# Kernel optimization log

Measured on AMD Instinct MI355X. Metric: run time of the kernel, lower is better.

The kernel has to match this reference:

```python
import jax, jax.numpy as jnp
import numpy as np

IN_F = 1024
OUT_F = 1024
GRID = 8
TOKENS = 8192


def setup_inputs() -> dict:
    key = jax.random.key(0)
    k_x, k_w, k_b, k_s = jax.random.split(key, 4)
    x = jax.random.normal(k_x, (TOKENS, IN_F), dtype=jnp.float32)
    # kaiming_uniform_(nonlinearity='linear'): bound = sqrt(3/fan_in)
    bound_w = float(np.sqrt(3.0 / IN_F))
    W = jax.random.uniform(k_w, (OUT_F, IN_F), minval=-bound_w, maxval=bound_w, dtype=jnp.float32)
    # nn.Linear default bias init: U(-1/sqrt(fan_in), 1/sqrt(fan_in))
    bound_b = float(1.0 / np.sqrt(IN_F))
    b = jax.random.uniform(k_b, (OUT_F,), minval=-bound_b, maxval=bound_b, dtype=jnp.float32)
    spline_weight = jax.random.uniform(k_s, (OUT_F, IN_F, GRID), minval=-0.1, maxval=0.1, dtype=jnp.float32)
    grid = jnp.linspace(-3.0, 3.0, GRID, dtype=jnp.float32)
    return {"x": x, "W": W, "b": b, "spline_weight": spline_weight, "grid": grid}


def reference(x, W, b, spline_weight, grid):
    grid_size = spline_weight.shape[-1]
    # base path: Linear(silu(x))
    base = jnp.einsum('ti,oi->to', jax.nn.silu(x), W) + b
    # RBF basis: [tokens, in_features, grid_size]
    denom = 2.0 / (grid_size - 1) + 1e-05
    basis = jnp.exp(-(((x[..., None] - grid) / denom) ** 2))
    spline = jnp.einsum('tig,oig->to', basis, spline_weight)
    return base + spline
```

## Files before the change

kernel.cpp:

```cpp
#include <hip/hip_runtime.h>
#include <hip/hip_bf16.h>

#define IN_F   1024
#define OUT_F  1024
#define GRID_N 8
#define TOKENS 8192
#define KTOT   9216
#define KHALF  4608
#define NTILE  72

typedef __attribute__((ext_vector_type(8))) short  bf16x8;
typedef __attribute__((ext_vector_type(4))) float  f32x4;

struct TrueT  { static constexpr bool value = true;  };
struct FalseT { static constexpr bool value = false; };

__device__ __forceinline__ unsigned int f2bf(float f) {
    union { float f; unsigned int u; } v; v.f = f;
    unsigned int r = v.u + 0x7fffu + ((v.u >> 16) & 1u);
    return r >> 16;
}

__global__ __launch_bounds__(256)
void prep_a_kernel(const float* __restrict__ x, const float* __restrict__ grid,
                   unsigned short* __restrict__ A)
{
    int idx = blockIdx.x * blockDim.x + threadIdx.x;
    int t = idx >> 10;
    int i = idx & 1023;
    float xv = x[idx];
    float sil = xv / (1.0f + __expf(-xv));
    A[(size_t)t * KTOT + i] = (unsigned short)f2bf(sil);

    const float invd = 1.0f / (2.0f / 7.0f + 1e-5f);
    unsigned int h[8];
    #pragma unroll
    for (int g = 0; g < 8; ++g) {
        float d = (xv - grid[g]) * invd;
        h[g] = f2bf(__expf(-d * d));
    }
    uint4 pk;
    pk.x = h[0] | (h[1] << 16);
    pk.y = h[2] | (h[3] << 16);
    pk.z = h[4] | (h[5] << 16);
    pk.w = h[6] | (h[7] << 16);
    *reinterpret_cast<uint4*>(&A[(size_t)t * KTOT + IN_F + (size_t)i * 8]) = pk;
}

__global__ __launch_bounds__(256)
void prep_b_kernel(const float* __restrict__ W, const float* __restrict__ spl,
                   unsigned short* __restrict__ B)
{
    int idx = blockIdx.x * blockDim.x + threadIdx.x;
    int o  = idx / (KTOT / 8);
    int c8 = idx - o * (KTOT / 8);
    const float* src = (c8 < IN_F / 8)
        ? (W   + (size_t)o * IN_F            + (size_t)c8 * 8)
        : (spl + (size_t)o * (IN_F * GRID_N) + (size_t)(c8 - IN_F / 8) * 8);
    const float4* s4 = reinterpret_cast<const float4*>(src);
    float4 lo = s4[0], hi = s4[1];
    uint4 pk;
    pk.x = f2bf(lo.x) | (f2bf(lo.y) << 16);
    pk.y = f2bf(lo.z) | (f2bf(lo.w) << 16);
    pk.z = f2bf(hi.x) | (f2bf(hi.y) << 16);
    pk.w = f2bf(hi.z) | (f2bf(hi.w) << 16);
    *reinterpret_cast<uint4*>(&B[(size_t)o * KTOT + (size_t)c8 * 8]) = pk;
}

#define GLOAD(src, dst) __builtin_amdgcn_global_load_lds( \
    (const __attribute__((address_space(1))) void*)(src),  \
    (__attribute__((address_space(3))) void*)(dst), 16, 0, 0)
#define SBAR()  __builtin_amdgcn_s_barrier()
#define SCH0()  __builtin_amdgcn_sched_barrier(0)
#define LGKM0() asm volatile("s_waitcnt lgkmcnt(0)" ::: "memory")
#define VMC0()  asm volatile("s_waitcnt vmcnt(0)" ::: "memory")

__global__ __launch_bounds__(512, 2)
void gemm_kan2(const unsigned short* __restrict__ A,
               const unsigned short* __restrict__ B,
               float* __restrict__ P, int rows)
{
    __shared__ char lds[131072];

    const int bid  = blockIdx.x;
    const int sk   = bid & 1;
    const int bn   = (bid >> 1) & 3;
    const int bm   = bid >> 3;
    const int tid  = threadIdx.x;
    const int wave = tid >> 6, lane = tid & 63;
    const int wr   = wave >> 2, wc = wave & 3;
    const int row  = lane & 15, kg = lane >> 4;
    const int sw   = row & 7;
    const int koff[2] = { (kg ^ sw) * 16, ((4 | kg) ^ sw) * 16 };
    const int l3 = lane >> 3, l7 = lane & 7;
    const int ksrc = (l7 ^ l3) * 8;
    const int k0 = sk * KHALF;

    const unsigned short* gA[4];
    const unsigned short* gB[4];
    #pragma unroll
    for (int r = 0; r < 4; ++r) {
        gA[r] = A + (size_t)(bm * 256 + wave * 32 + r * 8 + l3) * KTOT + k0 + ksrc;
        gB[r] = B + (size_t)(bn * 256 + wave * 32 + r * 8 + l3) * KTOT + k0 + ksrc;
    }

    f32x4 acc[8][4];
    const f32x4 zero = {0.f, 0.f, 0.f, 0.f};
    #pragma unroll
    for (int m = 0; m < 8; ++m)
        #pragma unroll
        for (int n = 0; n < 4; ++n) acc[m][n] = zero;

    {
        char* dA = lds + wave * 4096;
        char* dB = lds + 32768 + wave * 4096;
        #pragma unroll
        for (int r = 0; r < 4; ++r) GLOAD(gA[r], dA + r * 1024);
        #pragma unroll
        for (int r = 0; r < 4; ++r) GLOAD(gB[r], dB + r * 1024);
        #pragma unroll
        for (int r = 0; r < 4; ++r) { gA[r] += 64; gB[r] += 64; }
    }
    VMC0(); SBAR(); SCH0();

    const int aB = (wr * 128 + row) * 128;
    const int bB = 32768 + (wc * 64 + row) * 128;

    bf16x8 af[4][2], bf[2][2];
    int u = 0;

    auto tile = [&](auto stC) {
        constexpr bool ST = decltype(stC)::value;
        char* bufc = lds + (u & 1) * 65536;
        char* bufn = lds + ((u & 1) ^ 1) * 65536;

        #pragma unroll
        for (int mi = 0; mi < 4; ++mi)
            #pragma unroll
            for (int ks = 0; ks < 2; ++ks)
                af[mi][ks] = *(const bf16x8*)(bufc + aB + mi * 2048 + koff[ks]);
        #pragma unroll
        for (int ni = 0; ni < 2; ++ni)
            #pragma unroll
            for (int ks = 0; ks < 2; ++ks)
                bf[ni][ks] = *(const bf16x8*)(bufc + bB + ni * 2048 + koff[ks]);
        if constexpr (ST) {
            #pragma unroll
            for (int r = 0; r < 4; ++r)
                GLOAD(gA[r], bufn + wave * 4096 + r * 1024);
        }
        SBAR(); SCH0(); LGKM0(); SCH0();
        __builtin_amdgcn_s_setprio(1);
        #pragma unroll
        for (int mi = 0; mi < 4; ++mi)
            #pragma unroll
            for (int ni = 0; ni < 2; ++ni)
                #pragma unroll
                for (int ks = 0; ks < 2; ++ks)
                    acc[mi][ni] = __builtin_amdgcn_mfma_f32_16x16x32_bf16(
                        af[mi][ks], bf[ni][ks], acc[mi][ni], 0, 0, 0);
        __builtin_amdgcn_s_setprio(0);
        SBAR(); SCH0();

        #pragma unroll
        for (int ni = 0; ni < 2; ++ni)
            #pragma unroll
            for (int ks = 0; ks < 2; ++ks)
                bf[ni][ks] = *(const bf16x8*)(bufc + bB + (2 + ni) * 2048 + koff[ks]);
        if constexpr (ST) {
            #pragma unroll
            for (int r = 0; r < 2; ++r)
                GLOAD(gB[r], bufn + 32768 + wave * 4096 + r * 1024);
        }
        SBAR(); SCH0(); LGKM0(); SCH0();
        __builtin_amdgcn_s_setprio(1);
        #pragma unroll
        for (int mi = 0; mi < 4; ++mi)
            #pragma unroll
            for (int ni = 0; ni < 2; ++ni)
                #pragma unroll
                for (int ks = 0; ks < 2; ++ks)
                    acc[mi][2 + ni] = __builtin_amdgcn_mfma_f32_16x16x32_bf16(
                        af[mi][ks], bf[ni][ks], acc[mi][2 + ni], 0, 0, 0);
        __builtin_amdgcn_s_setprio(0);
        SBAR(); SCH0();

        #pragma unroll
        for (int mi = 0; mi < 4; ++mi)
            #pragma unroll
            for (int ks = 0; ks < 2; ++ks)
                af[mi][ks] = *(const bf16x8*)(bufc + aB + (4 + mi) * 2048 + koff[ks]);
        #pragma unroll
        for (int ni = 0; ni < 2; ++ni)
            #pragma unroll
            for (int ks = 0; ks < 2; ++ks)
                bf[ni][ks] = *(const bf16x8*)(bufc + bB + ni * 2048 + koff[ks]);
        if constexpr (ST) {
            #pragma unroll
            for (int r = 2; r < 4; ++r)
                GLOAD(gB[r], bufn + 32768 + wave * 4096 + r * 1024);
        }
        SBAR(); SCH0(); LGKM0(); SCH0();
        __builtin_amdgcn_s_setprio(1);
        #pragma unroll
        for (int mi = 0; mi < 4; ++mi)
            #pragma unroll
            for (int ni = 0; ni < 2; ++ni)
                #pragma unroll
                for (int ks = 0; ks < 2; ++ks)
                    acc[4 + mi][ni] = __builtin_amdgcn_mfma_f32_16x16x32_bf16(
                        af[mi][ks], bf[ni][ks], acc[4 + mi][ni], 0, 0, 0);
        __builtin_amdgcn_s_setprio(0);
        SBAR(); SCH0();

        #pragma unroll
        for (int ni = 0; ni < 2; ++ni)
            #pragma unroll
            for (int ks = 0; ks < 2; ++ks)
                bf[ni][ks] = *(const bf16x8*)(bufc + bB + (2 + ni) * 2048 + koff[ks]);
        SBAR(); SCH0(); LGKM0(); SCH0();
        __builtin_amdgcn_s_setprio(1);
        #pragma unroll
        for (int mi = 0; mi < 4; ++mi)
            #pragma unroll
            for (int ni = 0; ni < 2; ++ni)
                #pragma unroll
                for (int ks = 0; ks < 2; ++ks)
                    acc[4 + mi][2 + ni] = __builtin_amdgcn_mfma_f32_16x16x32_bf16(
                        af[mi][ks], bf[ni][ks], acc[4 + mi][2 + ni], 0, 0, 0);
        __builtin_amdgcn_s_setprio(0);
        VMC0();
        SBAR(); SCH0();

        if constexpr (ST) {
            #pragma unroll
            for (int r = 0; r < 4; ++r) { gA[r] += 64; gB[r] += 64; }
        }
    };

    for (u = 0; u < NTILE - 1; ++u) tile(TrueT{});
    tile(FalseT{});

    float* Pp = P + (size_t)sk * rows * OUT_F;
    const size_t orow0 = (size_t)bm * 256 + (size_t)wr * 128;
    const int    ocol0 = bn * 256 + wc * 64;
    #pragma unroll
    for (int n = 0; n < 4; ++n) {
        const int col = ocol0 + n * 16 + row;
        #pragma unroll
        for (int m = 0; m < 8; ++m) {
            #pragma unroll
            for (int j = 0; j < 4; ++j)
                Pp[(orow0 + m * 16 + kg * 4 + j) * OUT_F + col] = acc[m][n][j];
        }
    }
}

__global__ __launch_bounds__(256)
void reduce_kan(const float* __restrict__ P, const float* __restrict__ bias,
                float* __restrict__ out, int n4, int skStride4)
{
    const float4* p0 = (const float4*)P;
    const float4* p1 = p0 + skStride4;
    const float4* bv = (const float4*)bias;
    float4* o = (float4*)out;
    for (int i = blockIdx.x * blockDim.x + threadIdx.x; i < n4;
         i += gridDim.x * blockDim.x) {
        float4 a = p0[i], b = p1[i], c = bv[i & 255];
        float4 r;
        r.x = a.x + b.x + c.x;  r.y = a.y + b.y + c.y;
        r.z = a.z + b.z + c.z;  r.w = a.w + b.w + c.w;
        o[i] = r;
    }
}

extern "C" void kernel_launch(void* const* d_in, const int* in_sizes, int n_in,
                              void* d_out, int out_size, void* d_ws, size_t ws_size,
                              hipStream_t stream)
{
    const float* x    = (const float*)d_in[0];
    const float* W    = (const float*)d_in[1];
    const float* bias = (const float*)d_in[2];
    const float* spl  = (const float*)d_in[3];
    const float* grid = (const float*)d_in[4];
    float* out = (float*)d_out;

    unsigned short* Bw = (unsigned short*)d_ws;
    unsigned short* Aw = Bw + (size_t)OUT_F * KTOT;

    const size_t bBytes = (size_t)OUT_F * KTOT * 2;
    size_t avail = ws_size > bBytes ? ws_size - bBytes : 0;
    long maxRows = (long)(avail / 26624);
    int chunk = (maxRows >= TOKENS) ? TOKENS : (int)((maxRows / 256) * 256);
    if (chunk < 256) chunk = 256;
    float* Pp = (float*)(Aw + (size_t)chunk * KTOT);

    prep_b_kernel<<<(OUT_F * (KTOT / 8)) / 256, 256, 0, stream>>>(W, spl, Bw);

    for (int t0 = 0; t0 < TOKENS; t0 += chunk) {
        int rows = (TOKENS - t0 < chunk) ? (TOKENS - t0) : chunk;
        prep_a_kernel<<<(rows * IN_F) / 256, 256, 0, stream>>>(
            x + (size_t)t0 * IN_F, grid, Aw);
        gemm_kan2<<<(rows >> 8) * 8, 512, 0, stream>>>(Aw, Bw, Pp, rows);
        int n4 = rows * 256;
        int rblocks = (n4 + 255) / 256; if (rblocks > 2048) rblocks = 2048;
        reduce_kan<<<rblocks, 256, 0, stream>>>(
            Pp, bias, out + (size_t)t0 * OUT_F, n4, n4);
    }
}
```

Measured before the change: 203.6 us.

## Issue all next-tile loads upfront with partial vmcnt waits and remap LDS layout

All eight global-to-LDS loads for the next K tile are now issued at the start of each tile instead of being spread over three phases. Partial vmcnt waits let the first half of the buffer become usable before the rest has landed. Each thread now loads rows tid>>3 plus multiples of 64, so the LDS rows are regrouped into 64-row halves, and the wave-to-output mapping and epilogue indexing change to match. The goal is deeper memory-level parallelism and fewer full vmcnt(0) stalls, at the cost of more in-flight loads and a more complex ordering that the vmcnt values must get exactly right.

After: 215.9 us. 1.06x slower.

```diff
diff --git a/kernel.cpp b/kernel.cpp
--- a/kernel.cpp
+++ b/kernel.cpp
@@ -73,7 +73,7 @@
 #define SBAR()  __builtin_amdgcn_s_barrier()
 #define SCH0()  __builtin_amdgcn_sched_barrier(0)
 #define LGKM0() asm volatile("s_waitcnt lgkmcnt(0)" ::: "memory")
-#define VMC0()  asm volatile("s_waitcnt vmcnt(0)" ::: "memory")
+#define VMCNT_(n) asm volatile("s_waitcnt vmcnt(" #n ")" ::: "memory")
 
 __global__ __launch_bounds__(512, 2)
 void gemm_kan2(const unsigned short* __restrict__ A,
@@ -89,20 +89,16 @@
     const int tid  = threadIdx.x;
     const int wave = tid >> 6, lane = tid & 63;
     const int wr   = wave >> 2, wc = wave & 3;
-    const int row  = lane & 15, kg = lane >> 4;
-    const int sw   = row & 7;
+    const int fr   = lane & 15, kg = lane >> 4;
+    const int sw   = fr & 7;
     const int koff[2] = { (kg ^ sw) * 16, ((4 | kg) ^ sw) * 16 };
-    const int l3 = lane >> 3, l7 = lane & 7;
-    const int ksrc = (l7 ^ l3) * 8;
     const int k0 = sk * KHALF;
 
-    const unsigned short* gA[4];
-    const unsigned short* gB[4];
-    #pragma unroll
-    for (int r = 0; r < 4; ++r) {
-        gA[r] = A + (size_t)(bm * 256 + wave * 32 + r * 8 + l3) * KTOT + k0 + ksrc;
-        gB[r] = B + (size_t)(bn * 256 + wave * 32 + r * 8 + l3) * KTOT + k0 + ksrc;
-    }
+    const int trow = tid >> 3;
+    const int ksrc = ((tid & 7) ^ (trow & 7)) * 8;
+    const unsigned short* gA = A + (size_t)(bm * 256 + trow) * KTOT + k0 + ksrc;
+    const unsigned short* gB = B + (size_t)(bn * 256 + trow) * KTOT + k0 + ksrc;
+    const size_t R64 = (size_t)64 * KTOT;
 
     f32x4 acc[8][4];
     const f32x4 zero = {0.f, 0.f, 0.f, 0.f};
@@ -112,19 +108,17 @@
         for (int n = 0; n < 4; ++n) acc[m][n] = zero;
 
     {
-        char* dA = lds + wave * 4096;
-        char* dB = lds + 32768 + wave * 4096;
-        #pragma unroll
-        for (int r = 0; r < 4; ++r) GLOAD(gA[r], dA + r * 1024);
-        #pragma unroll
-        for (int r = 0; r < 4; ++r) GLOAD(gB[r], dB + r * 1024);
-        #pragma unroll
-        for (int r = 0; r < 4; ++r) { gA[r] += 64; gB[r] += 64; }
-    }
-    VMC0(); SBAR(); SCH0();
-
-    const int aB = (wr * 128 + row) * 128;
-    const int bB = 32768 + (wc * 64 + row) * 128;
+        char* d = lds + tid * 16;
+        GLOAD(gA,           d);            GLOAD(gA + R64,     d + 8192);
+        GLOAD(gB,           d + 32768);    GLOAD(gB + R64,     d + 40960);
+        GLOAD(gB + 2 * R64, d + 49152);    GLOAD(gB + 3 * R64, d + 57344);
+        GLOAD(gA + 2 * R64, d + 16384);    GLOAD(gA + 3 * R64, d + 24576);
+        gA += 64; gB += 64;
+    }
+    VMCNT_(4); SBAR(); SCH0();
+
+    const int aOff = (wr * 64 + fr) * 128;
+    const int bOff = 32768 + (wc * 32 + fr) * 128;
 
     bf16x8 af[4][2], bf[2][2];
     int u = 0;
@@ -132,22 +126,26 @@
     auto tile = [&](auto stC) {
         constexpr bool ST = decltype(stC)::value;
         char* bufc = lds + (u & 1) * 65536;
-        char* bufn = lds + ((u & 1) ^ 1) * 65536;
-
-        #pragma unroll
-        for (int mi = 0; mi < 4; ++mi)
-            #pragma unroll
-            for (int ks = 0; ks < 2; ++ks)
-                af[mi][ks] = *(const bf16x8*)(bufc + aB + mi * 2048 + koff[ks]);
-        #pragma unroll
-        for (int ni = 0; ni < 2; ++ni)
-            #pragma unroll
-            for (int ks = 0; ks < 2; ++ks)
-                bf[ni][ks] = *(const bf16x8*)(bufc + bB + ni * 2048 + koff[ks]);
+
+        #pragma unroll
+        for (int mi = 0; mi < 4; ++mi)
+            #pragma unroll
+            for (int ks = 0; ks < 2; ++ks)
+                af[mi][ks] = *(const bf16x8*)(bufc + aOff + mi * 2048 + koff[ks]);
+        #pragma unroll
+        for (int ni = 0; ni < 2; ++ni)
+            #pragma unroll
+            for (int ks = 0; ks < 2; ++ks)
+                bf[ni][ks] = *(const bf16x8*)(bufc + bOff + ni * 2048 + koff[ks]);
         if constexpr (ST) {
-            #pragma unroll
-            for (int r = 0; r < 4; ++r)
-                GLOAD(gA[r], bufn + wave * 4096 + r * 1024);
+            char* d = lds + ((u & 1) ^ 1) * 65536 + tid * 16;
+            GLOAD(gA,           d);            GLOAD(gA + R64,     d + 8192);
+            GLOAD(gB,           d + 32768);    GLOAD(gB + R64,     d + 40960);
+            GLOAD(gB + 2 * R64, d + 49152);    GLOAD(gB + 3 * R64, d + 57344);
+            GLOAD(gA + 2 * R64, d + 16384);    GLOAD(gA + 3 * R64, d + 24576);
+            VMCNT_(8);
+        } else {
+            VMCNT_(0);
         }
         SBAR(); SCH0(); LGKM0(); SCH0();
         __builtin_amdgcn_s_setprio(1);
@@ -166,12 +164,7 @@
         for (int ni = 0; ni < 2; ++ni)
             #pragma unroll
             for (int ks = 0; ks < 2; ++ks)
-                bf[ni][ks] = *(const bf16x8*)(bufc + bB + (2 + ni) * 2048 + koff[ks]);
-        if constexpr (ST) {
-            #pragma unroll
-            for (int r = 0; r < 2; ++r)
-                GLOAD(gB[r], bufn + 32768 + wave * 4096 + r * 1024);
-        }
+                bf[ni][ks] = *(const bf16x8*)(bufc + bOff + 16384 + ni * 2048 + koff[ks]);
         SBAR(); SCH0(); LGKM0(); SCH0();
         __builtin_amdgcn_s_setprio(1);
         #pragma unroll
@@ -189,17 +182,12 @@
         for (int mi = 0; mi < 4; ++mi)
             #pragma unroll
             for (int ks = 0; ks < 2; ++ks)
-                af[mi][ks] = *(const bf16x8*)(bufc + aB + (4 + mi) * 2048 + koff[ks]);
-        #pragma unroll
-        for (int ni = 0; ni < 2; ++ni)
-            #pragma unroll
-            for (int ks = 0; ks < 2; ++ks)
-                bf[ni][ks] = *(const bf16x8*)(bufc + bB + ni * 2048 + koff[ks]);
-        if constexpr (ST) {
-            #pragma unroll
-            for (int r = 2; r < 4; ++r)
-                GLOAD(gB[r], bufn + 32768 + wave * 4096 + r * 1024);
-        }
+                af[mi][ks] = *(const bf16x8*)(bufc + aOff + 16384 + mi * 2048 + koff[ks]);
+        #pragma unroll
+        for (int ni = 0; ni < 2; ++ni)
+            #pragma unroll
+            for (int ks = 0; ks < 2; ++ks)
+                bf[ni][ks] = *(const bf16x8*)(bufc + bOff + ni * 2048 + koff[ks]);
         SBAR(); SCH0(); LGKM0(); SCH0();
         __builtin_amdgcn_s_setprio(1);
         #pragma unroll
@@ -217,7 +205,10 @@
         for (int ni = 0; ni < 2; ++ni)
             #pragma unroll
             for (int ks = 0; ks < 2; ++ks)
-                bf[ni][ks] = *(const bf16x8*)(bufc + bB + (2 + ni) * 2048 + koff[ks]);
+                bf[ni][ks] = *(const bf16x8*)(bufc + bOff + 16384 + ni * 2048 + koff[ks]);
+        if constexpr (ST) {
+            VMCNT_(4);
+        }
         SBAR(); SCH0(); LGKM0(); SCH0();
         __builtin_amdgcn_s_setprio(1);
         #pragma unroll
@@ -229,29 +220,26 @@
                     acc[4 + mi][2 + ni] = __builtin_amdgcn_mfma_f32_16x16x32_bf16(
                         af[mi][ks], bf[ni][ks], acc[4 + mi][2 + ni], 0, 0, 0);
         __builtin_amdgcn_s_setprio(0);
-        VMC0();
-        SBAR(); SCH0();
-
-        if constexpr (ST) {
-            #pragma unroll
-            for (int r = 0; r < 4; ++r) { gA[r] += 64; gB[r] += 64; }
-        }
+        SBAR(); SCH0();
+
+        if constexpr (ST) { gA += 64; gB += 64; }
     };
 
     for (u = 0; u < NTILE - 1; ++u) tile(TrueT{});
     tile(FalseT{});
 
     float* Pp = P + (size_t)sk * rows * OUT_F;
-    const size_t orow0 = (size_t)bm * 256 + (size_t)wr * 128;
-    const int    ocol0 = bn * 256 + wc * 64;
+    const size_t orow0 = (size_t)bm * 256 + (size_t)wr * 64;
+    const int    ocol0 = bn * 256 + wc * 32;
     #pragma unroll
     for (int n = 0; n < 4; ++n) {
-        const int col = ocol0 + n * 16 + row;
+        const int col = ocol0 + (n & 1) * 16 + (n >> 1) * 128 + fr;
         #pragma unroll
         for (int m = 0; m < 8; ++m) {
+            const size_t r0 = orow0 + (m & 3) * 16 + (m >> 2) * 128 + kg * 4;
             #pragma unroll
             for (int j = 0; j < 4; ++j)
-                Pp[(orow0 + m * 16 + kg * 4 + j) * OUT_F + col] = acc[m][n][j];
+                Pp[(r0 + j) * OUT_F + col] = acc[m][n][j];
         }
     }
 }
```
